# Performance work log

Measured on AMD Instinct MI355X. Metric: run time of the kernel, lower is better.

The kernel has to match this reference:

```python
import jax, jax.numpy as jnp
import numpy as np

B, S, DIM = 2, 2048, 4096
NH, NKV, HD = 32, 8, 128          # head_dim = dim // n_heads
BLOCK = 16                         # paged-cache block size
NBLK_PER_SEQ = S // BLOCK          # 128
NUM_BLOCKS = B * NBLK_PER_SEQ      # 256 physical blocks
SCALE = 1.0 / np.sqrt(HD).astype(np.float32)


def _rope(x, fc):
    # x: [B,S,H,HD]; fc: [S,1,HD//2,2] (cos,sin) -- matches apply_rotary_emb
    xr = x.astype(jnp.float32).reshape(*x.shape[:-1], HD // 2, 2)
    cos, sin = fc[..., 0], fc[..., 1]
    out = jnp.stack([xr[..., 0] * cos - xr[..., 1] * sin,
                     xr[..., 1] * cos + xr[..., 0] * sin], axis=-1)
    return out.reshape(x.shape).astype(x.dtype)


def setup_inputs() -> dict:
    key = jax.random.key(0)
    ks = jax.random.split(key, 3)
    x = jax.random.normal(ks[0], (B, S, DIM), jnp.float32)
    wqkv_w = jax.random.normal(ks[1], ((NH + 2 * NKV) * HD, DIM), jnp.float32) * (DIM ** -0.5)
    wo_w = jax.random.normal(ks[2], (DIM, DIM), jnp.float32) * (DIM ** -0.5)
    # rotary table: [S, 1, HD/2, 2] so it broadcasts over (B, S, H, HD/2)
    pos = jnp.arange(S, dtype=jnp.float32)
    inv = 10000.0 ** (-jnp.arange(0, HD, 2, dtype=jnp.float32) / HD)
    ang = pos[:, None] * inv[None, :]
    freqs_cis = jnp.stack([jnp.cos(ang), jnp.sin(ang)], -1)[:, None, :, :]
    k_cache = jnp.zeros((NUM_BLOCKS, BLOCK, NKV, HD), jnp.float32)
    v_cache = jnp.zeros((NUM_BLOCKS, BLOCK, NKV, HD), jnp.float32)
    block_table = jnp.arange(B * NBLK_PER_SEQ, dtype=jnp.int32).reshape(B, NBLK_PER_SEQ)
    seqlens_k = jnp.full((B,), S, jnp.int32)
    return {"x": x, "wqkv_w": wqkv_w, "wo_w": wo_w, "freqs_cis": freqs_cis,
            "k_cache": k_cache, "v_cache": v_cache,
            "block_table": block_table, "seqlens_k": seqlens_k}


def reference(x, wqkv_w, wo_w, freqs_cis, k_cache, v_cache, block_table, seqlens_k):
    # fused QKV projection
    qkv = x @ wqkv_w.T                                   # [B,S,(NH+2*NKV)*HD]
    q, k, v = jnp.split(qkv, [NH * HD, (NH + NKV) * HD], axis=-1)
    q = q.reshape(B, S, NH, HD)
    k = k.reshape(B, S, NKV, HD)
    v = v.reshape(B, S, NKV, HD)
    q = _rope(q, freqs_cis)
    k = _rope(k, freqs_cis)
    # paged KV-cache write (prefill): slot = block_table[b, t//BLOCK]*BLOCK + t%BLOCK
    t = jnp.arange(S)
    slots = block_table[:, t // BLOCK] * BLOCK + (t % BLOCK)[None, :]    # [B,S]
    flat = slots.reshape(-1)
    kc = k_cache.reshape(NUM_BLOCKS * BLOCK, NKV, HD).at[flat].set(k.reshape(B * S, NKV, HD))
    vc = v_cache.reshape(NUM_BLOCKS * BLOCK, NKV, HD).at[flat].set(v.reshape(B * S, NKV, HD))
    # block-table indexed attention: gather K/V back through the page table
    kk = kc[slots]                                       # [B,S,NKV,HD]
    vv = vc[slots]                                       # [B,S,NKV,HD]
    G = NH // NKV                                        # GQA group size
    qg = q.reshape(B, S, NKV, G, HD)
    scores = jnp.einsum('bqkgd,bskd->bkgqs', qg, kk) * SCALE  # [B,NKV,G,S,S]
    qpos = jnp.arange(S)[:, None]
    kpos = jnp.arange(S)[None, :]
    causal = kpos <= qpos                                # [S,S]
    valid = kpos[None] < seqlens_k[:, None, None]        # [B,S,S]
    mask = (causal[None] & valid)[:, None, None]         # [B,1,1,S,S]
    scores = jnp.where(mask, scores, -jnp.inf)
    p = jax.nn.softmax(scores, axis=-1)
    attn = jnp.einsum('bkgqs,bskd->bqkgd', p, vv).reshape(B, S, NH * HD)
    return attn @ wo_w.T
```

## Files before the change

### kernel.cpp

```cpp
#include <hip/hip_runtime.h>
#include <hip/hip_fp16.h>

typedef _Float16 f16;
typedef _Float16 f16x4 __attribute__((ext_vector_type(4)));
typedef _Float16 f16x8 __attribute__((ext_vector_type(8)));
typedef float    f32x4 __attribute__((ext_vector_type(4)));

#define NEG_INF (-__builtin_inff())
#define AS1 __attribute__((address_space(1)))
#define AS3 __attribute__((address_space(3)))
#define GLOAD_LDS16(g, l) \
    __builtin_amdgcn_global_load_lds((AS1 const void*)(g), (AS3 void*)(l), 16, 0, 0)
#define BARRIER() do { asm volatile("" ::: "memory"); \
                       __builtin_amdgcn_s_barrier(); \
                       asm volatile("" ::: "memory"); } while (0)

__global__ __launch_bounds__(256) void cvt_f32_f16(const float* __restrict__ in,
                                                   f16* __restrict__ out, int n4) {
    int i = blockIdx.x * 256 + threadIdx.x;
    if (i >= n4) return;
    float4 v = ((const float4*)in)[i];
    f16x4 h = {(f16)v.x, (f16)v.y, (f16)v.z, (f16)v.w};
    ((f16x4*)out)[i] = h;
}

template <typename CT>
__global__ __launch_bounds__(512) void gemm256(const f16* __restrict__ A,
                                               const f16* __restrict__ Bt,
                                               CT* __restrict__ C,
                                               int M, int N, int K) {
    __shared__ __align__(16) f16 smem[65536];
    f16* LA = smem;
    f16* LB = smem + 32768;

    const int tid  = threadIdx.x;
    const int wave = tid >> 6, lane = tid & 63;
    const int quad = lane >> 4, m16 = lane & 15;
    const int wm = wave >> 2, wn = wave & 3;

    const int ntn = N >> 8;
    const int nwg = (M >> 8) * ntn;
    const int q8 = nwg >> 3, r8 = nwg & 7;
    const int xcd = blockIdx.x & 7, idx = blockIdx.x >> 3;
    const int swz = (xcd < r8 ? xcd * (q8 + 1) : r8 * (q8 + 1) + (xcd - r8) * q8) + idx;
    const int bm = (swz / ntn) << 8;
    const int bn = (swz % ntn) << 8;

    const int rowW = tid >> 3;
    const int gsrc = (tid & 7) ^ (rowW & 7);
    const f16* gA0 = A  + (size_t)(bm + rowW) * K + gsrc * 8;
    const f16* gA1 = A  + (size_t)(bm + 128 + rowW) * K + gsrc * 8;
    const f16* gB0 = Bt + (size_t)(bn + rowW) * K + gsrc * 8;
    const f16* gB1 = Bt + (size_t)(bn + 128 + rowW) * K + gsrc * 8;
    const size_t rstep = (size_t)64 * K;
    const int lw = wave * 512;

#define STG(dstbase, gp, kt) do { \
    GLOAD_LDS16((gp) + (size_t)(kt) * 64,         (dstbase) + lw); \
    GLOAD_LDS16((gp) + (size_t)(kt) * 64 + rstep, (dstbase) + lw + 4096); } while (0)

    int foff[2];
#pragma unroll
    for (int ks = 0; ks < 2; ++ks)
        foff[ks] = (((ks << 2) | quad) ^ (m16 & 7)) * 8;
    const int arow = wm * 8192 + m16 * 64;
    const int brow = (wn >> 1) * 8192 + (wn & 1) * 4096 + m16 * 64;

    f32x4 acc[8][4];
#pragma unroll
    for (int i = 0; i < 8; ++i)
#pragma unroll
        for (int j = 0; j < 4; ++j)
#pragma unroll
            for (int e = 0; e < 4; ++e) acc[i][j][e] = 0.f;

    const int NT = K >> 6;

    STG(LA, gA0, 0); STG(LA + 8192, gA1, 0);
    STG(LB, gB0, 0); STG(LB + 8192, gB1, 0);
    STG(LB + 16384, gB0, 1); STG(LB + 16384 + 8192, gB1, 1);
    asm volatile("s_waitcnt vmcnt(4)" ::: "memory");
    BARRIER();

    f16x8 af[4][2], bf0[2][2], bf1[2][2];

    for (int t = 0; t < NT; ++t) {
        const int bo = (t & 1) * 16384;
        const f16* pa = LA + bo + arow;
        const f16* pb = LB + bo + brow;

#pragma unroll
        for (int mt = 0; mt < 4; ++mt)
#pragma unroll
            for (int ks = 0; ks < 2; ++ks)
                af[mt][ks] = *(const f16x8*)(pa + mt * 1024 + foff[ks]);
#pragma unroll
        for (int nt = 0; nt < 2; ++nt)
#pragma unroll
            for (int ks = 0; ks < 2; ++ks)
                bf0[nt][ks] = *(const f16x8*)(pb + nt * 1024 + foff[ks]);
        if (t + 1 < NT) STG(LA + (bo ^ 16384), gA0, t + 1);
        BARRIER();
        asm volatile("s_waitcnt lgkmcnt(0)" ::: "memory");
        __builtin_amdgcn_s_setprio(1);
#pragma unroll
        for (int mt = 0; mt < 4; ++mt)
#pragma unroll
            for (int nt = 0; nt < 2; ++nt)
#pragma unroll
                for (int ks = 0; ks < 2; ++ks)
                    acc[mt][nt] = __builtin_amdgcn_mfma_f32_16x16x32_f16(
                        af[mt][ks], bf0[nt][ks], acc[mt][nt], 0, 0, 0);
        __builtin_amdgcn_s_setprio(0);
        BARRIER();

#pragma unroll
        for (int nt = 0; nt < 2; ++nt)
#pragma unroll
            for (int ks = 0; ks < 2; ++ks)
                bf1[nt][ks] = *(const f16x8*)(pb + (nt + 2) * 1024 + foff[ks]);
        if (t + 1 < NT) STG(LA + (bo ^ 16384) + 8192, gA1, t + 1);
        BARRIER();
        asm volatile("s_waitcnt lgkmcnt(0)" ::: "memory");
        __builtin_amdgcn_s_setprio(1);
#pragma unroll
        for (int mt = 0; mt < 4; ++mt)
#pragma unroll
            for (int nt = 0; nt < 2; ++nt)
#pragma unroll
                for (int ks = 0; ks < 2; ++ks)
                    acc[mt][nt + 2] = __builtin_amdgcn_mfma_f32_16x16x32_f16(
                        af[mt][ks], bf1[nt][ks], acc[mt][nt + 2], 0, 0, 0);
        __builtin_amdgcn_s_setprio(0);
        BARRIER();

#pragma unroll
        for (int mt = 0; mt < 4; ++mt)
#pragma unroll
            for (int ks = 0; ks < 2; ++ks)
                af[mt][ks] = *(const f16x8*)(pa + (mt + 4) * 1024 + foff[ks]);
        if (t + 2 < NT) STG(LB + bo, gB0, t + 2);
        BARRIER();
        asm volatile("s_waitcnt lgkmcnt(0)" ::: "memory");
        __builtin_amdgcn_s_setprio(1);
#pragma unroll
        for (int mt = 0; mt < 4; ++mt)
#pragma unroll
            for (int nt = 0; nt < 2; ++nt)
#pragma unroll
                for (int ks = 0; ks < 2; ++ks)
                    acc[mt + 4][nt + 2] = __builtin_amdgcn_mfma_f32_16x16x32_f16(
                        af[mt][ks], bf1[nt][ks], acc[mt + 4][nt + 2], 0, 0, 0);
        __builtin_amdgcn_s_setprio(0);
        BARRIER();

        if (t + 2 < NT) STG(LB + bo + 8192, gB1, t + 2);
        BARRIER();
        __builtin_amdgcn_s_setprio(1);
#pragma unroll
        for (int mt = 0; mt < 4; ++mt)
#pragma unroll
            for (int nt = 0; nt < 2; ++nt)
#pragma unroll
                for (int ks = 0; ks < 2; ++ks)
                    acc[mt + 4][nt] = __builtin_amdgcn_mfma_f32_16x16x32_f16(
                        af[mt][ks], bf0[nt][ks], acc[mt + 4][nt], 0, 0, 0);
        __builtin_amdgcn_s_setprio(0);
        if (t + 2 < NT) { asm volatile("s_waitcnt vmcnt(4)" ::: "memory"); }
        else            { asm volatile("s_waitcnt vmcnt(0)" ::: "memory"); }
        BARRIER();
    }
#undef STG

#pragma unroll
    for (int mt = 0; mt < 8; ++mt)
#pragma unroll
        for (int r = 0; r < 4; ++r) {
            int row = bm + wm * 128 + mt * 16 + quad * 4 + r;
            CT* cp = C + (size_t)row * N + bn + wn * 64 + m16;
#pragma unroll
            for (int nt = 0; nt < 4; ++nt) cp[nt * 16] = (CT)acc[mt][nt][r];
        }
}

__global__ __launch_bounds__(256) void rope_qk(const f16* __restrict__ qkv,
                                               const float* __restrict__ freqs,
                                               f16* __restrict__ qh,
                                               f16* __restrict__ kk) {
    int idx  = blockIdx.x * 256 + threadIdx.x;
    int row  = idx / 2560;
    int p    = idx - row * 2560;
    int b    = row >> 11, s = row & 2047;
    int head = p >> 6, i = p & 63;
    const f16* src = qkv + (size_t)row * 6144 + head * 128 + 2 * i;
    float v0 = (float)src[0], v1 = (float)src[1];
    float c  = freqs[s * 128 + 2 * i];
    float sn = freqs[s * 128 + 2 * i + 1];
    float r0 = v0 * c - v1 * sn;
    float r1 = v1 * c + v0 * sn;
    f16* dst = (head < 32)
        ? qh + (((size_t)(b * 32 + head)) * 2048 + s) * 128 + 2 * i
        : kk + (((size_t)(b * 8 + head - 32)) * 2048 + s) * 128 + 2 * i;
    dst[0] = (f16)r0; dst[1] = (f16)r1;
}

__global__ __launch_bounds__(256) void transpose_v(const f16* __restrict__ qkv,
                                                   f16* __restrict__ vvt) {
    __shared__ f16 T[64][72];
    const int st = blockIdx.x, dt = blockIdx.y;
    const int b = blockIdx.z >> 3, kvh = blockIdx.z & 7;
    const int tid = threadIdx.x;
    const int sr = tid >> 3, c8 = (tid & 7) * 8;
#pragma unroll
    for (int rep = 0; rep < 2; ++rep) {
        int sl = rep * 32 + sr;
        *(f16x8*)&T[sl][c8] =
            *(const f16x8*)(qkv + (size_t)(b * 2048 + st * 64 + sl) * 6144
                            + 5120 + kvh * 128 + dt * 64 + c8);
    }
    __syncthreads();
#pragma unroll
    for (int rep = 0; rep < 2; ++rep) {
        int dl = rep * 32 + sr;
        f16x8 v;
#pragma unroll
        for (int j = 0; j < 8; ++j) v[j] = T[c8 + j][dl];
        *(f16x8*)(vvt + (((size_t)(b * 8 + kvh)) * 128 + dt * 64 + dl) * 2048
                  + st * 64 + c8) = v;
    }
}

__global__ __launch_bounds__(256) void attn_fused(const f16* __restrict__ qh,
                                                  const f16* __restrict__ kk,
                                                  const f16* __restrict__ vvt,
                                                  const int* __restrict__ seqlens,
                                                  f16* __restrict__ out) {
    __shared__ f16 KsPs[64 * 136];
    __shared__ f16 Vs[128][72];
    const int pair = blockIdx.x;
    const int h = blockIdx.y, b = blockIdx.z;
    const int kvh = h >> 2;
    const int tid = threadIdx.x, wave = tid >> 6, lane = tid & 63;
    const int quad = lane >> 4, m16 = lane & 15;
    f16* Ps = KsPs;

    const int seqlen = seqlens[b];
    const f16* kbp = kk  + ((size_t)(b * 8 + kvh) * 2048) * 128;
    const f16* vbp = vvt + ((size_t)(b * 8 + kvh) * 128) * 2048;

    for (int half = 0; half < 2; ++half) {
        const int qt = half ? pair : (31 - pair);
        const int qbase = qt * 64;
        const int qw = qbase + wave * 16;

        const f16* qptr = qh + (((size_t)(b * 32 + h)) * 2048 + qw + m16) * 128;
        f16x8 qf[4];
#pragma unroll
        for (int c = 0; c < 4; ++c) qf[c] = *(const f16x8*)(qptr + c * 32 + quad * 8);

        float m_i[4], l_i[4];
        f32x4 oacc[8];
#pragma unroll
        for (int r = 0; r < 4; ++r) { m_i[r] = NEG_INF; l_i[r] = 0.f; }
#pragma unroll
        for (int dt = 0; dt < 8; ++dt)
#pragma unroll
            for (int e = 0; e < 4; ++e) oacc[dt][e] = 0.f;

        int kmax = qbase + 64; if (seqlen < kmax) kmax = seqlen;

        for (int kt = 0; kt < kmax; kt += 64) {
            __syncthreads();
#pragma unroll
            for (int it = 0; it < 4; ++it) {
                int g = it * 256 + tid;
                int r_ = g >> 4, c8 = (g & 15) * 8;
                *(f16x8*)&KsPs[r_ * 136 + c8] = *(const f16x8*)(kbp + (size_t)(kt + r_) * 128 + c8);
            }
#pragma unroll
            for (int it = 0; it < 4; ++it) {
                int g = it * 256 + tid;
                int r_ = g >> 3, c8 = (g & 7) * 8;
                *(f16x8*)&Vs[r_][c8] = *(const f16x8*)(vbp + (size_t)r_ * 2048 + kt + c8);
            }
            __syncthreads();

            f32x4 sc[4];
#pragma unroll
            for (int nt = 0; nt < 4; ++nt) {
                f32x4 s = {0.f, 0.f, 0.f, 0.f};
#pragma unroll
                for (int c = 0; c < 4; ++c) {
                    f16x8 kf = *(const f16x8*)&KsPs[(nt * 16 + m16) * 136 + c * 32 + quad * 8];
                    s = __builtin_amdgcn_mfma_f32_16x16x32_f16(qf[c], kf, s, 0, 0, 0);
                }
                sc[nt] = s;
            }

            float sv[4][4];
            float mt[4] = {NEG_INF, NEG_INF, NEG_INF, NEG_INF};
#pragma unroll
            for (int nt = 0; nt < 4; ++nt) {
                int kpos = kt + nt * 16 + m16;
#pragma unroll
                for (int r = 0; r < 4; ++r) {
                    int qpos = qw + quad * 4 + r;
                    float sx = sc[nt][r] * 0.08838834764831845f;
                    sx = (kpos <= qpos && kpos < seqlen) ? sx : NEG_INF;
                    sv[nt][r] = sx;
                    mt[r] = fmaxf(mt[r], sx);
                }
            }
#pragma unroll
            for (int off = 1; off < 16; off <<= 1)
#pragma unroll
                for (int r = 0; r < 4; ++r)
                    mt[r] = fmaxf(mt[r], __shfl_xor(mt[r], off, 64));

            float alpha[4], mm[4];
#pragma unroll
            for (int r = 0; r < 4; ++r) {
                float mo = m_i[r];
                float mn = fmaxf(mo, mt[r]);
                float mmr = fmaxf(mn, -1e30f);
                alpha[r] = __expf(mo - mmr);
                m_i[r] = mn;
                mm[r] = mmr;
            }
            float rs[4] = {0.f, 0.f, 0.f, 0.f};
#pragma unroll
            for (int nt = 0; nt < 4; ++nt)
#pragma unroll
                for (int r = 0; r < 4; ++r) {
                    float pv = __expf(sv[nt][r] - mm[r]);
                    sv[nt][r] = pv;
                    rs[r] += pv;
                }
#pragma unroll
            for (int off = 1; off < 16; off <<= 1)
#pragma unroll
                for (int r = 0; r < 4; ++r) rs[r] += __shfl_xor(rs[r], off, 64);
#pragma unroll
            for (int r = 0; r < 4; ++r) l_i[r] = l_i[r] * alpha[r] + rs[r];
#pragma unroll
            for (int dt = 0; dt < 8; ++dt)
#pragma unroll
                for (int r = 0; r < 4; ++r) oacc[dt][r] *= alpha[r];

            __syncthreads();

#pragma unroll
            for (int nt = 0; nt < 4; ++nt)
#pragma unroll
                for (int r = 0; r < 4; ++r)
                    Ps[(wave * 16 + quad * 4 + r) * 72 + nt * 16 + m16] = (f16)sv[nt][r];

            f16x8 pf[2];
#pragma unroll
            for (int c = 0; c < 2; ++c)
                pf[c] = *(const f16x8*)&Ps[(wave * 16 + m16) * 72 + c * 32 + quad * 8];
#pragma unroll
            for (int dt = 0; dt < 8; ++dt)
#pragma unroll
                for (int c = 0; c < 2; ++c) {
                    f16x8 vf = *(const f16x8*)&Vs[dt * 16 + m16][c * 32 + quad * 8];
                    oacc[dt] = __builtin_amdgcn_mfma_f32_16x16x32_f16(pf[c], vf, oacc[dt], 0, 0, 0);
                }
        }

#pragma unroll
        for (int r = 0; r < 4; ++r) {
            int qpos = qw + quad * 4 + r;
            float inv = 1.0f / l_i[r];
            f16* op = out + ((size_t)b * 2048 + qpos) * 4096 + h * 128;
#pragma unroll
            for (int dt = 0; dt < 8; ++dt)
                op[dt * 16 + m16] = (f16)(oacc[dt][r] * inv);
        }
    }
}

extern "C" void kernel_launch(void* const* d_in, const int* in_sizes, int n_in,
                              void* d_out, int out_size, void* d_ws, size_t ws_size,
                              hipStream_t stream) {
    const float* x     = (const float*)d_in[0];
    const float* wqkv  = (const float*)d_in[1];
    const float* wo    = (const float*)d_in[2];
    const float* freqs = (const float*)d_in[3];
    const int*   seql  = (const int*)d_in[7];
    float* out = (float*)d_out;

    char* ws = (char*)d_ws;
    size_t o = 0;
    f16* xh    = (f16*)(ws + o); o += (size_t)4096 * 4096 * 2;
    f16* wqkvh = (f16*)(ws + o); o += (size_t)6144 * 4096 * 2;
    f16* woh   = (f16*)(ws + o); o += (size_t)4096 * 4096 * 2;
    f16* qkvh  = (f16*)(ws + o); o += (size_t)4096 * 6144 * 2;
    f16* qhp   = (f16*)(ws + o); o += (size_t)4096 * 4096 * 2;
    f16* kkp   = (f16*)(ws + o); o += (size_t)4096 * 8 * 128 * 2;
    f16* vvt   = (f16*)(ws + o); o += (size_t)4096 * 8 * 128 * 2;
    f16* attnh = xh;

    cvt_f32_f16<<<16384, 256, 0, stream>>>(x, xh, 4194304);
    cvt_f32_f16<<<24576, 256, 0, stream>>>(wqkv, wqkvh, 6291456);
    cvt_f32_f16<<<16384, 256, 0, stream>>>(wo, woh, 4194304);

    gemm256<f16><<<384, 512, 0, stream>>>(xh, wqkvh, qkvh, 4096, 6144, 4096);

    rope_qk<<<40960, 256, 0, stream>>>(qkvh, freqs, qhp, kkp);
    transpose_v<<<dim3(32, 2, 16), 256, 0, stream>>>(qkvh, vvt);

    attn_fused<<<dim3(16, 32, 2), 256, 0, stream>>>(qhp, kkp, vvt, seql, attnh);

    gemm256<float><<<256, 512, 0, stream>>>(attnh, woh, out, 4096, 4096, 4096);
}
```

Measured before the change: 842.3 us.

## Prefetch next K/V tile into registers, use exp2 softmax and skip rescale

The attention kernel now loads the next 64-row K and V tile from global memory into registers while the current tile is being computed, so global latency overlaps with the MFMA and softmax work. The scale is folded together with log2(e) so the softmax can use the hardware exp2 instruction. The rescale of the output accumulators and running sum is skipped when no row max grows, and __syncthreads is replaced with raw barriers plus an explicit lgkmcnt wait. The price is higher register pressure from the eight f16x8 prefetch registers, plus a wave-divergent branch around the rescale.

```diff
diff --git a/kernel.cpp b/kernel.cpp
--- a/kernel.cpp
+++ b/kernel.cpp
@@ -11,6 +11,7 @@
 #define AS3 __attribute__((address_space(3)))
 #define GLOAD_LDS16(g, l) \
     __builtin_amdgcn_global_load_lds((AS1 const void*)(g), (AS3 void*)(l), 16, 0, 0)
+#define EXP2F(x) __builtin_amdgcn_exp2f(x)
 #define BARRIER() do { asm volatile("" ::: "memory"); \
                        __builtin_amdgcn_s_barrier(); \
                        asm volatile("" ::: "memory"); } while (0)
@@ -248,6 +249,8 @@
     const f16* kbp = kk  + ((size_t)(b * 8 + kvh) * 2048) * 128;
     const f16* vbp = vvt + ((size_t)(b * 8 + kvh) * 128) * 2048;
 
+    const float SCL2 = 0.08838834764831845f * 1.4426950408889634f;
+
     for (int half = 0; half < 2; ++half) {
         const int qt = half ? pair : (31 - pair);
         const int qbase = qt * 64;
@@ -269,21 +272,32 @@
 
         int kmax = qbase + 64; if (seqlen < kmax) kmax = seqlen;
 
+        f16x8 gk[4], gv[4];
+#pragma unroll
+        for (int it = 0; it < 4; ++it) {
+            int g = it * 256 + tid;
+            gk[it] = *(const f16x8*)(kbp + (size_t)(g >> 4) * 128 + (g & 15) * 8);
+            gv[it] = *(const f16x8*)(vbp + (size_t)(g >> 3) * 2048 + (g & 7) * 8);
+        }
+
         for (int kt = 0; kt < kmax; kt += 64) {
-            __syncthreads();
+            BARRIER();
 #pragma unroll
             for (int it = 0; it < 4; ++it) {
                 int g = it * 256 + tid;
-                int r_ = g >> 4, c8 = (g & 15) * 8;
-                *(f16x8*)&KsPs[r_ * 136 + c8] = *(const f16x8*)(kbp + (size_t)(kt + r_) * 128 + c8);
+                *(f16x8*)&KsPs[(g >> 4) * 136 + (g & 15) * 8] = gk[it];
+                *(f16x8*)&Vs[g >> 3][(g & 7) * 8] = gv[it];
             }
-#pragma unroll
-            for (int it = 0; it < 4; ++it) {
-                int g = it * 256 + tid;
-                int r_ = g >> 3, c8 = (g & 7) * 8;
-                *(f16x8*)&Vs[r_][c8] = *(const f16x8*)(vbp + (size_t)r_ * 2048 + kt + c8);
+            if (kt + 64 < kmax) {
+#pragma unroll
+                for (int it = 0; it < 4; ++it) {
+                    int g = it * 256 + tid;
+                    gk[it] = *(const f16x8*)(kbp + (size_t)(kt + 64 + (g >> 4)) * 128 + (g & 15) * 8);
+                    gv[it] = *(const f16x8*)(vbp + (size_t)(g >> 3) * 2048 + (kt + 64) + (g & 7) * 8);
+                }
             }
-            __syncthreads();
+            asm volatile("s_waitcnt lgkmcnt(0)" ::: "memory");
+            BARRIER();
 
             f32x4 sc[4];
 #pragma unroll
@@ -305,7 +319,7 @@
 #pragma unroll
                 for (int r = 0; r < 4; ++r) {
                     int qpos = qw + quad * 4 + r;
-                    float sx = sc[nt][r] * 0.08838834764831845f;
+                    float sx = sc[nt][r] * SCL2;
                     sx = (kpos <= qpos && kpos < seqlen) ? sx : NEG_INF;
                     sv[nt][r] = sx;
                     mt[r] = fmaxf(mt[r], sx);
@@ -317,22 +331,32 @@
                 for (int r = 0; r < 4; ++r)
                     mt[r] = fmaxf(mt[r], __shfl_xor(mt[r], off, 64));
 
-            float alpha[4], mm[4];
-#pragma unroll
-            for (int r = 0; r < 4; ++r) {
-                float mo = m_i[r];
-                float mn = fmaxf(mo, mt[r]);
-                float mmr = fmaxf(mn, -1e30f);
-                alpha[r] = __expf(mo - mmr);
-                m_i[r] = mn;
-                mm[r] = mmr;
+            float mm[4];
+            bool grow = (mt[0] > m_i[0]) | (mt[1] > m_i[1]) |
+                        (mt[2] > m_i[2]) | (mt[3] > m_i[3]);
+            if (grow) {
+#pragma unroll
+                for (int r = 0; r < 4; ++r) {
+                    float mo = m_i[r];
+                    float mn = fmaxf(mo, mt[r]);
+                    float mmr = fmaxf(mn, -1e30f);
+                    float a = EXP2F(mo - mmr);
+                    m_i[r] = mn;
+                    mm[r] = mmr;
+                    l_i[r] *= a;
+#pragma unroll
+                    for (int dt = 0; dt < 8; ++dt) oacc[dt][r] *= a;
+                }
+            } else {
+#pragma unroll
+                for (int r = 0; r < 4; ++r) mm[r] = fmaxf(m_i[r], -1e30f);
             }
             float rs[4] = {0.f, 0.f, 0.f, 0.f};
 #pragma unroll
             for (int nt = 0; nt < 4; ++nt)
 #pragma unroll
                 for (int r = 0; r < 4; ++r) {
-                    float pv = __expf(sv[nt][r] - mm[r]);
+                    float pv = EXP2F(sv[nt][r] - mm[r]);
                     sv[nt][r] = pv;
                     rs[r] += pv;
                 }
@@ -341,13 +365,9 @@
 #pragma unroll
                 for (int r = 0; r < 4; ++r) rs[r] += __shfl_xor(rs[r], off, 64);
 #pragma unroll
-            for (int r = 0; r < 4; ++r) l_i[r] = l_i[r] * alpha[r] + rs[r];
-#pragma unroll
-            for (int dt = 0; dt < 8; ++dt)
-#pragma unroll
-                for (int r = 0; r < 4; ++r) oacc[dt][r] *= alpha[r];
-
-            __syncthreads();
+            for (int r = 0; r < 4; ++r) l_i[r] += rs[r];
+
+            BARRIER();
 
 #pragma unroll
             for (int nt = 0; nt < 4; ++nt)
```

Result: no change. 830.0 us (-1.5%).
